# Performance work log

Hardware: AMD Instinct MI355X
Metric: run time of the kernel (lower is better)

## Reference

```python
import jax, jax.numpy as jnp
import numpy as np

HEADS = 8


def setup_inputs() -> dict:
    key = jax.random.key(0)
    ks = jax.random.split(key, 12)
    B, H, W, C = 2, 128, 256, 256
    inner = C  # num_heads * dim_head = 8 * 32

    def p(k, shape):
        return jax.random.normal(k, shape, dtype=jnp.float32) * 0.02

    return {
        "x": jax.random.normal(ks[0], (B, H * W, C), dtype=jnp.float32),
        "Wq_h": p(ks[1], (C, inner)),
        "Wk_h": p(ks[2], (C, inner)),
        "Wv_h": p(ks[3], (C, inner)),
        "Wo_h": p(ks[4], (inner, C)),
        "bo_h": p(ks[5], (C,)),
        "Wq_w": p(ks[6], (C, inner)),
        "Wk_w": p(ks[7], (C, inner)),
        "Wv_w": p(ks[8], (C, inner)),
        "Wo_w": p(ks[9], (inner, C)),
        "bo_w": p(ks[10], (C,)),
        "h": H,
        "w": W,
    }


def reference(x, Wq_h, Wk_h, Wv_h, Wo_h, bo_h, Wq_w, Wk_w, Wv_w, Wo_w, bo_w, h, w):
    b, n, c = x.shape
    heads = HEADS
    d = Wq_h.shape[1] // heads  # dim_head
    scale = d ** -0.5
    xs = x.reshape(b, h, w, c)  # [B,H,W,C]

    def proj(Wm):
        # [B,H,W,heads,d]
        return (xs @ Wm).reshape(b, h, w, heads, d)

    # --- height-axis attention: each column attends across all rows ---
    q, k, v = proj(Wq_h), proj(Wk_h), proj(Wv_h)
    s = jnp.einsum('bxwnd,bywnd->bwnxy', q, k) * scale  # [B,W,heads,H,H]
    a = jax.nn.softmax(s, axis=-1)
    oh = jnp.einsum('bwnxy,bywnd->bxwnd', a, v).reshape(b, h, w, heads * d)
    oh = oh @ Wo_h + bo_h

    # --- width-axis attention: each row attends across all columns ---
    q, k, v = proj(Wq_w), proj(Wk_w), proj(Wv_w)
    s = jnp.einsum('bhxnd,bhynd->bhnxy', q, k) * scale  # [B,H,heads,W,W]
    a = jax.nn.softmax(s, axis=-1)
    ow = jnp.einsum('bhnxy,bhynd->bhxnd', a, v).reshape(b, h, w, heads * d)
    ow = ow @ Wo_w + bo_w

    return (oh + ow).reshape(b, n, c)
```

## Files before the change

### kernel.cpp

```cpp
#include <hip/hip_runtime.h>
#include <hip/hip_bf16.h>
#include <stdint.h>

typedef unsigned short u16;
typedef short bf16x8 __attribute__((ext_vector_type(8)));
typedef float f32x4  __attribute__((ext_vector_type(4)));
typedef float f32x16 __attribute__((ext_vector_type(16)));
typedef unsigned int u32x4 __attribute__((ext_vector_type(4)));

__device__ __forceinline__ u16 f2bf(float f) {
    uint32_t u = __builtin_bit_cast(uint32_t, f);
    u += 0x7fffu + ((u >> 16) & 1u);
    return (u16)(u >> 16);
}

#if __has_builtin(__builtin_amdgcn_exp2f)
#define EXP2(x) __builtin_amdgcn_exp2f(x)
#else
extern "C" __device__ float __ocml_native_exp2_f32(float);
#define EXP2(x) __ocml_native_exp2_f32(x)
#endif

__device__ __forceinline__ void gl_lds16(const u16* g, u16* l) {
    __builtin_amdgcn_global_load_lds(
        (__attribute__((address_space(1))) void*)(g),
        (__attribute__((address_space(3))) void*)(l),
        16, 0, 0);
}

#define MM 65536
#define CC 256

#define QSCALE (1.4426950408889634f * 0.17677669529663687f)

__device__ __forceinline__ int perm_h(int t) {
    return ((t >> 15) << 15) | ((t & 127) << 8) | ((t >> 7) & 255);
}


__global__ void prep_kernel(
    const float* __restrict__ Wq_h, const float* __restrict__ Wk_h, const float* __restrict__ Wv_h,
    const float* __restrict__ Wo_h, const float* __restrict__ bo_h,
    const float* __restrict__ Wq_w, const float* __restrict__ Wk_w, const float* __restrict__ Wv_w,
    const float* __restrict__ Wo_w, const float* __restrict__ bo_w,
    u16* __restrict__ Wh_t, u16* __restrict__ Ww_t,
    u16* __restrict__ Woh_t, u16* __restrict__ Wow_t,
    u16* __restrict__ Wocat, float* __restrict__ bias)
{
    const int tid = blockIdx.x * 256 + threadIdx.x;
    const int nth = gridDim.x * 256;

    for (int i = tid; i < 768 * 256; i += nth) {
        int n = i >> 8, kk = i & 255;
        int which = n >> 8, nn = n & 255;
        const float* Wsh = (which == 0) ? Wq_h : (which == 1) ? Wk_h : Wv_h;
        const float* Wsw = (which == 0) ? Wq_w : (which == 1) ? Wk_w : Wv_w;
        Wh_t[i] = f2bf(Wsh[kk * 256 + nn]);
        Ww_t[i] = f2bf(Wsw[kk * 256 + nn]);
    }
    for (int i = tid; i < 256 * 256; i += nth) {
        int n = i >> 8, k = i & 255;
        Woh_t[i] = f2bf(Wo_h[k * 256 + n]);
        Wow_t[i] = f2bf(Wo_w[k * 256 + n]);
    }
    for (int i = tid; i < 256 * 512; i += nth) {
        int n = i >> 9, k = i & 511;
        float v = (k < 256) ? Wo_h[k * 256 + n] : Wo_w[(k - 256) * 256 + n];
        Wocat[i] = f2bf(v);
    }
    for (int i = tid; i < 256; i += nth) bias[i] = bo_h[i] + bo_w[i];
}

__global__ __launch_bounds__(256) void xcvt_kernel(const float* __restrict__ x, u16* __restrict__ xb)
{
    int i = blockIdx.x * 256 + threadIdx.x;
    const int nth = gridDim.x * 256;
    const int total = MM * 256 / 8;
    for (; i < total; i += nth) {
        const float* ap = x + (size_t)i * 8;
        float4 f0 = *(const float4*)ap;
        float4 f1 = *(const float4*)(ap + 4);
        u16 o[8] = { f2bf(f0.x), f2bf(f0.y), f2bf(f0.z), f2bf(f0.w),
                     f2bf(f1.x), f2bf(f1.y), f2bf(f1.z), f2bf(f1.w) };
        *(int4*)(xb + (size_t)i * 8) = *(const int4*)o;
    }
}

template<int PH, int XB>
__global__ __launch_bounds__(256) void gemm_qk_kernel(
    const float* __restrict__ x, const u16* __restrict__ xb, const u16* __restrict__ Bt,
    u16* __restrict__ Qb, u16* __restrict__ Kb)
{
    constexpr int S = PH ? 128 : 256;
    constexpr int L = PH ? 7 : 8;
    const int K = 256;
    __shared__ u16 sh[XB ? 32768 : 16384];
    const int tid = threadIdx.x;
    const int lane = tid & 63, wave = tid >> 6;
    const int wm = wave & 1, wn = wave >> 1;
    const int l15 = lane & 15, lq = lane >> 4;

    const int id = blockIdx.x;
    const int xcd = id & 7, wq = id >> 3;
    const int mt = xcd * 64 + (wq >> 2), nt = wq & 3;
    const int m0 = mt * 128, n0 = nt * 128;

    f32x4 acc[4][4];
#pragma unroll
    for (int i = 0; i < 4; i++)
#pragma unroll
        for (int j = 0; j < 4; j++)
#pragma unroll
            for (int t = 0; t < 4; t++) acc[i][j][t] = 0.0f;

    auto mma_tile = [&](const u16* As, const u16* Bs) {
#pragma unroll
        for (int ks = 0; ks < 2; ks++) {
            bf16x8 af[4], bfr[4];
#pragma unroll
            for (int i = 0; i < 4; i++) {
                int row = wm * 64 + i * 16 + l15;
                int ca  = ks * 4 + lq;
                af[i]  = *(const bf16x8*)(As + row * 64 + ((ca ^ (row & 7)) << 3));
                int nn  = wn * 64 + i * 16 + l15;
                bfr[i] = *(const bf16x8*)(Bs + nn * 64 + ((ca ^ (nn & 7)) << 3));
            }
#pragma unroll
            for (int i = 0; i < 4; i++)
#pragma unroll
                for (int j = 0; j < 4; j++)
                    acc[i][j] = __builtin_amdgcn_mfma_f32_16x16x32_bf16(af[i], bfr[j], acc[i][j], 0, 0, 0);
        }
    };

    if constexpr (XB) {
        u16* As_[2] = { sh,        sh + 16384 };
        u16* Bs_[2] = { sh + 8192, sh + 24576 };
        auto stage = [&](int kt, int buf) {
#pragma unroll
            for (int i = 0; i < 4; i++) {
                int cid = i * 256 + tid;
                int r = cid >> 3, sc = cid & 7;
                int gk = kt + ((sc ^ (r & 7)) << 3);
                int rm = PH ? perm_h(m0 + r) : (m0 + r);
                gl_lds16(xb + (size_t)rm * 256 + gk, As_[buf] + cid * 8);
                gl_lds16(Bt + (size_t)(n0 + r) * K + gk, Bs_[buf] + cid * 8);
            }
        };
        stage(0, 0);
        __syncthreads();
#pragma unroll
        for (int t = 0; t < 4; t++) {
            if (t + 1 < 4) stage((t + 1) * 64, (t + 1) & 1);
            mma_tile(As_[t & 1], Bs_[t & 1]);
            __syncthreads();
        }
    } else {
        u16* As = sh;
        u16* Bs = sh + 8192;
        for (int kt = 0; kt < K; kt += 64) {
            __syncthreads();
#pragma unroll
            for (int i = 0; i < 4; i++) {
                int cid = i * 256 + tid;
                int r = cid >> 3, sc = cid & 7;
                int gk = kt + ((sc ^ (r & 7)) << 3);
                int rm = PH ? perm_h(m0 + r) : (m0 + r);
                const float* ap = x + (size_t)rm * 256 + gk;
                float4 f0 = *(const float4*)ap;
                float4 f1 = *(const float4*)(ap + 4);
                u16 o[8] = { f2bf(f0.x), f2bf(f0.y), f2bf(f0.z), f2bf(f0.w),
                             f2bf(f1.x), f2bf(f1.y), f2bf(f1.z), f2bf(f1.w) };
                *(int4*)(As + (size_t)cid * 8) = *(const int4*)o;
                *(int4*)(Bs + (size_t)cid * 8) = *(const int4*)(Bt + (size_t)(n0 + r) * K + gk);
            }
            __syncthreads();
            mma_tile(As, Bs);
        }
        __syncthreads();
    }

    const float scale = (nt < 2) ? (float)QSCALE : 1.0f;
#pragma unroll
    for (int i = 0; i < 4; i++)
#pragma unroll
        for (int j = 0; j < 4; j++)
#pragma unroll
            for (int r = 0; r < 4; r++) {
                int row = wm * 64 + i * 16 + lq * 4 + r;
                int col = wn * 64 + j * 16 + l15;
                sh[row * 128 + (col ^ ((row & 7) << 3))] = f2bf(acc[i][j][r] * scale);
            }
    __syncthreads();

    u16* dstb = (nt < 2) ? Qb : Kb;
    const int head = (nt * 4 + wave) & 7;
    const int gi = m0 >> L;
    const int seqbase = m0 & (S - 1);
    u16* dst = dstb + ((size_t)(gi * 8 + head) * S + seqbase) * 32;
    const int ln_ = lane & 31, lh_ = lane >> 5;
#pragma unroll
    for (int qt = 0; qt < 4; qt++)
#pragma unroll
        for (int half = 0; half < 2; half++) {
            int row  = qt * 32 + ln_;
            int colb = wave * 32 + half * 16 + lh_ * 8;
            int4 v = *(const int4*)(sh + row * 128 + (colb ^ ((row & 7) << 3)));
            *(int4*)(dst + qt * 1024 + half * 512 + lane * 8) = v;
        }
}

template<int PH, int XB>
__global__ __launch_bounds__(256) void gemm_vt_kernel(
    const u16* __restrict__ Wt, const float* __restrict__ x, const u16* __restrict__ xb,
    u16* __restrict__ Vb)
{
    constexpr int S = PH ? 128 : 256;
    const int K = 256;
    __shared__ u16 sh[XB ? 32768 : 16384];
    const int tid = threadIdx.x;
    const int lane = tid & 63, wave = tid >> 6;
    const int wm = wave & 1, wn = wave >> 1;
    const int l15 = lane & 15, lq = lane >> 4;
    const int m0 = blockIdx.y * 128, n0 = blockIdx.x * 128;

    f32x4 acc[4][4];
#pragma unroll
    for (int i = 0; i < 4; i++)
#pragma unroll
        for (int j = 0; j < 4; j++)
#pragma unroll
            for (int t = 0; t < 4; t++) acc[i][j][t] = 0.0f;

    auto mma_tile = [&](const u16* As, const u16* Bs) {
#pragma unroll
        for (int ks = 0; ks < 2; ks++) {
            bf16x8 af[4], bfr[4];
#pragma unroll
            for (int i = 0; i < 4; i++) {
                int row = wm * 64 + i * 16 + l15;
                int ca  = ks * 4 + lq;
                af[i]  = *(const bf16x8*)(As + row * 64 + ((ca ^ (row & 7)) << 3));
                int nn  = wn * 64 + i * 16 + l15;
                bfr[i] = *(const bf16x8*)(Bs + nn * 64 + ((ca ^ (nn & 7)) << 3));
            }
#pragma unroll
            for (int i = 0; i < 4; i++)
#pragma unroll
                for (int j = 0; j < 4; j++)
                    acc[i][j] = __builtin_amdgcn_mfma_f32_16x16x32_bf16(af[i], bfr[j], acc[i][j], 0, 0, 0);
        }
    };

    if constexpr (XB) {
        u16* As_[2] = { sh,        sh + 16384 };
        u16* Bs_[2] = { sh + 8192, sh + 24576 };
        auto stage = [&](int kt, int buf) {
#pragma unroll
            for (int i = 0; i < 4; i++) {
                int cid = i * 256 + tid;
                int r = cid >> 3, sc = cid & 7;
                int gk = kt + ((sc ^ (r & 7)) << 3);
                gl_lds16(Wt + (size_t)(m0 + r) * K + gk, As_[buf] + cid * 8);
                int cm = PH ? perm_h(n0 + r) : (n0 + r);
                gl_lds16(xb + (size_t)cm * 256 + gk, Bs_[buf] + cid * 8);
            }
        };
        stage(0, 0);
        __syncthreads();
#pragma unroll
        for (int t = 0; t < 4; t++) {
            if (t + 1 < 4) stage((t + 1) * 64, (t + 1) & 1);
            mma_tile(As_[t & 1], Bs_[t & 1]);
            __syncthreads();
        }
    } else {
        u16* As = sh;
        u16* Bs = sh + 8192;
        for (int kt = 0; kt < K; kt += 64) {
            __syncthreads();
#pragma unroll
            for (int i = 0; i < 4; i++) {
                int cid = i * 256 + tid;
                int r = cid >> 3, sc = cid & 7;
                int gk = kt + ((sc ^ (r & 7)) << 3);
                *(int4*)(As + (size_t)cid * 8) = *(const int4*)(Wt + (size_t)(m0 + r) * K + gk);
                int cm = PH ? perm_h(n0 + r) : (n0 + r);
                const float* bp = x + (size_t)cm * 256 + gk;
                float4 f0 = *(const float4*)bp;
                float4 f1 = *(const float4*)(bp + 4);
                u16 o[8] = { f2bf(f0.x), f2bf(f0.y), f2bf(f0.z), f2bf(f0.w),
                             f2bf(f1.x), f2bf(f1.y), f2bf(f1.z), f2bf(f1.w) };
                *(int4*)(Bs + (size_t)cid * 8) = *(const int4*)o;
            }
            __syncthreads();
            mma_tile(As, Bs);
        }
        __syncthreads();
    }

#pragma unroll
    for (int i = 0; i < 4; i++)
#pragma unroll
        for (int j = 0; j < 4; j++)
#pragma unroll
            for (int r = 0; r < 4; r++) {
                int row = wm * 64 + i * 16 + lq * 4 + r;
                int col = wn * 64 + j * 16 + l15;
                sh[row * 128 + (col ^ ((row & 7) << 3))] = f2bf(acc[i][j][r]);
            }
    __syncthreads();

    const int gi = n0 >> (PH ? 7 : 8);
    const int seqbase = n0 & (S - 1);
    const int head = (m0 >> 5) + wave;
    u16* dst = Vb + ((size_t)(gi * 8 + head) * S + seqbase) * 32;
    const int ln_ = lane & 31, lh_ = lane >> 5;
#pragma unroll
    for (int cl = 0; cl < 4; cl++)
#pragma unroll
        for (int half = 0; half < 2; half++) {
            int row  = wave * 32 + ln_;
            int colb = cl * 32 + half * 16 + lh_ * 8;
            int4 v = *(const int4*)(sh + row * 128 + (colb ^ ((row & 7) << 3)));
            *(int4*)(dst + cl * 1024 + half * 512 + lane * 8) = v;
        }
}

__global__ __launch_bounds__(256) void gemm_out_fused_kernel(
    const u16* __restrict__ Ah, const u16* __restrict__ Aw,
    const u16* __restrict__ Bcat, float* __restrict__ Cout, const float* __restrict__ bias)
{
    const int K = 512, N = 256;
    __shared__ u16 sh[32768];
    const int tid = threadIdx.x;
    const int lane = tid & 63, wave = tid >> 6;
    const int wm = wave & 1, wn = wave >> 1;
    const int l15 = lane & 15, lq = lane >> 4;

    const int id = blockIdx.x;
    const int xcd = id & 7, wq = id >> 3;
    const int mt = xcd * 64 + (wq >> 1), nt = wq & 1;
    const int m0 = mt * 128, n0 = nt * 128;

    f32x4 acc[4][4];
#pragma unroll
    for (int i = 0; i < 4; i++)
#pragma unroll
        for (int j = 0; j < 4; j++)
#pragma unroll
            for (int t = 0; t < 4; t++) acc[i][j][t] = 0.0f;

    u16* As_[2] = { sh,        sh + 16384 };
    u16* Bs_[2] = { sh + 8192, sh + 24576 };
    auto stage = [&](int kt, int buf) {
        const u16* Abase = (kt < 256) ? Ah : Aw;
        int koff = kt & 255;
#pragma unroll
        for (int i = 0; i < 4; i++) {
            int cid = i * 256 + tid;
            int r = cid >> 3, sc = cid & 7;
            int gs = (sc ^ (r & 7)) << 3;
            gl_lds16(Abase + (size_t)(m0 + r) * 256 + koff + gs, As_[buf] + cid * 8);
            gl_lds16(Bcat + (size_t)(n0 + r) * K + kt + gs, Bs_[buf] + cid * 8);
        }
    };

    stage(0, 0);
    __syncthreads();
#pragma unroll
    for (int t = 0; t < 8; t++) {
        if (t + 1 < 8) stage((t + 1) * 64, (t + 1) & 1);
        const u16* As = As_[t & 1];
        const u16* Bs = Bs_[t & 1];
#pragma unroll
        for (int ks = 0; ks < 2; ks++) {
            bf16x8 af[4], bfr[4];
#pragma unroll
            for (int i = 0; i < 4; i++) {
                int row = wm * 64 + i * 16 + l15;
                int ca  = ks * 4 + lq;
                af[i]  = *(const bf16x8*)(As + row * 64 + ((ca ^ (row & 7)) << 3));
                int nn  = wn * 64 + i * 16 + l15;
                bfr[i] = *(const bf16x8*)(Bs + nn * 64 + ((ca ^ (nn & 7)) << 3));
            }
#pragma unroll
            for (int i = 0; i < 4; i++)
#pragma unroll
                for (int j = 0; j < 4; j++)
                    acc[i][j] = __builtin_amdgcn_mfma_f32_16x16x32_bf16(af[i], bfr[j], acc[i][j], 0, 0, 0);
        }
        __syncthreads();
    }
#pragma unroll
    for (int i = 0; i < 4; i++)
#pragma unroll
        for (int j = 0; j < 4; j++)
#pragma unroll
            for (int r = 0; r < 4; r++) {
                int row = m0 + wm * 64 + i * 16 + lq * 4 + r;
                int col = n0 + wn * 64 + j * 16 + l15;
                Cout[(size_t)row * N + col] = acc[i][j][r] + bias[col];
            }
}

template<int MODE>
__global__ __launch_bounds__(256) void gemm_out_kernel(
    const u16* __restrict__ A16, const u16* __restrict__ Bt,
    float* __restrict__ Cout, const float* __restrict__ bias)
{
    const int K = 256, N = 256;
    __shared__ u16 As[128 * 64];
    __shared__ u16 Bs[128 * 64];
    const int tid = threadIdx.x;
    const int lane = tid & 63, wave = tid >> 6;
    const int wm = wave & 1, wn = wave >> 1;
    const int l15 = lane & 15, lq = lane >> 4;
    const int m0 = blockIdx.y * 128, n0 = blockIdx.x * 128;

    f32x4 acc[4][4];
#pragma unroll
    for (int i = 0; i < 4; i++)
#pragma unroll
        for (int j = 0; j < 4; j++)
#pragma unroll
            for (int t = 0; t < 4; t++) acc[i][j][t] = 0.0f;

    for (int kt = 0; kt < K; kt += 64) {
        __syncthreads();
#pragma unroll
        for (int i = 0; i < 4; i++) {
            int cid = i * 256 + tid;
            int r = cid >> 3, sc = cid & 7;
            int gk = kt + ((sc ^ (r & 7)) << 3);
            *(int4*)(As + (size_t)cid * 8) = *(const int4*)(A16 + (size_t)(m0 + r) * K + gk);
            *(int4*)(Bs + (size_t)cid * 8) = *(const int4*)(Bt + (size_t)(n0 + r) * K + gk);
        }
        __syncthreads();
#pragma unroll
        for (int ks = 0; ks < 2; ks++) {
            bf16x8 af[4], bfr[4];
#pragma unroll
            for (int i = 0; i < 4; i++) {
                int row = wm * 64 + i * 16 + l15;
                int ca  = ks * 4 + lq;
                af[i]  = *(const bf16x8*)(As + row * 64 + ((ca ^ (row & 7)) << 3));
                int nn  = wn * 64 + i * 16 + l15;
                bfr[i] = *(const bf16x8*)(Bs + nn * 64 + ((ca ^ (nn & 7)) << 3));
            }
#pragma unroll
            for (int i = 0; i < 4; i++)
#pragma unroll
                for (int j = 0; j < 4; j++)
                    acc[i][j] = __builtin_amdgcn_mfma_f32_16x16x32_bf16(af[i], bfr[j], acc[i][j], 0, 0, 0);
        }
    }
#pragma unroll
    for (int i = 0; i < 4; i++)
#pragma unroll
        for (int j = 0; j < 4; j++)
#pragma unroll
            for (int r = 0; r < 4; r++) {
                int row = m0 + wm * 64 + i * 16 + lq * 4 + r;
                int col = n0 + wn * 64 + j * 16 + l15;
                size_t idx = (size_t)row * N + col;
                if (MODE == 1) Cout[idx] = acc[i][j][r] + bias[col];
                else           Cout[idx] += acc[i][j][r];
            }
}

template<int S, int PH, int NT>
__global__ __launch_bounds__(NT) void attn_kernel(
    const u16* __restrict__ Qb, const u16* __restrict__ Kb,
    const u16* __restrict__ Vb, u16* __restrict__ att)
{
    constexpr int NC = S / 32;
    const int tid = threadIdx.x;
    const int lane = tid & 63;
    const int wave = tid >> 6;
    const int ln = lane & 31;
    const int lh = lane >> 5;

    const int bid = blockIdx.x;
    const int head = bid & 7;
    const int gi = bid >> 3;
    const int qs = wave * 32;
    const int g = gi * 8 + head;

    const u16* Qg = Qb + (size_t)g * S * 32;
    const u16* Kg = Kb + (size_t)g * S * 32;
    const u16* Vg = Vb + (size_t)g * S * 32;

    const u16* qp = Qg + (qs >> 5) * 1024 + lane * 8;
    bf16x8 bq0 = *(const bf16x8*)qp;
    bf16x8 bq1 = *(const bf16x8*)(qp + 512);

    f32x16 kz;
#pragma unroll
    for (int t = 0; t < 16; t++) kz[t] = 0.0f;
    asm("" : "+v"(kz));

    float rs[4] = {0.0f, 0.0f, 0.0f, 0.0f};
    f32x16 oacc;
#pragma unroll
    for (int t = 0; t < 16; t++) oacc[t] = 0.0f;

    const u16* kp0 = Kg + lane * 8;
    const u16* vp0 = Vg + lane * 8;
    bf16x8 ak0 = *(const bf16x8*)kp0;
    bf16x8 ak1 = *(const bf16x8*)(kp0 + 512);
    bf16x8 bv0 = *(const bf16x8*)vp0;
    bf16x8 bv1 = *(const bf16x8*)(vp0 + 512);

    for (int c = 0; c < NC; c++) {
        f32x16 z = __builtin_amdgcn_mfma_f32_32x32x16_bf16(ak0, bq0, kz, 0, 0, 0);
        z = __builtin_amdgcn_mfma_f32_32x32x16_bf16(ak1, bq1, z, 0, 0, 0);

        int cn = (c + 1 < NC) ? c + 1 : c;
        const u16* kp = kp0 + cn * 1024;
        const u16* vp = vp0 + cn * 1024;
        bf16x8 nk0 = *(const bf16x8*)kp;
        bf16x8 nk1 = *(const bf16x8*)(kp + 512);
        bf16x8 nv0 = *(const bf16x8*)vp;
        bf16x8 nv1 = *(const bf16x8*)(vp + 512);

        asm("" : "+v"(z));
        float p[16];
#pragma unroll
        for (int r = 0; r < 16; r++) { p[r] = EXP2(z[r]); rs[r & 3] += p[r]; }

        unsigned w[8];
#pragma unroll
        for (int t = 0; t < 8; t++) {
            unsigned d;
            asm("v_cvt_pk_bf16_f32 %0, %1, %2" : "=v"(d) : "v"(p[2 * t]), "v"(p[2 * t + 1]));
            w[t] = d;
        }
        auto s0 = __builtin_amdgcn_permlane32_swap(w[0], w[2], false, false);
        auto s1 = __builtin_amdgcn_permlane32_swap(w[1], w[3], false, false);
        auto s2 = __builtin_amdgcn_permlane32_swap(w[4], w[6], false, false);
        auto s3 = __builtin_amdgcn_permlane32_swap(w[5], w[7], false, false);
        u32x4 a0 = { (unsigned)s0[0], (unsigned)s1[0], (unsigned)s0[1], (unsigned)s1[1] };
        u32x4 a1 = { (unsigned)s2[0], (unsigned)s3[0], (unsigned)s2[1], (unsigned)s3[1] };
        bf16x8 pa0 = __builtin_bit_cast(bf16x8, a0);
        bf16x8 pa1 = __builtin_bit_cast(bf16x8, a1);

        oacc = __builtin_amdgcn_mfma_f32_32x32x16_bf16(pa0, bv0, oacc, 0, 0, 0);
        oacc = __builtin_amdgcn_mfma_f32_32x32x16_bf16(pa1, bv1, oacc, 0, 0, 0);

        ak0 = nk0; ak1 = nk1; bv0 = nv0; bv1 = nv1;
    }

    float rsum = (rs[0] + rs[1]) + (rs[2] + rs[3]);
    rsum += __shfl_xor(rsum, 32);
    float inv = 1.0f / rsum;
#pragma unroll
    for (int r = 0; r < 16; r++) {
        int row = (r & 3) + ((r >> 2) << 3) + (lh << 2);
        float is = __shfl(inv, row);
        int seq = qs + row;
        int m = PH ? ((gi >> 8) * 32768 + seq * 256 + (gi & 255))
                   : (gi * 256 + seq);
        att[(size_t)m * 256 + head * 32 + ln] = f2bf(oacc[r] * is);
    }
}

extern "C" void kernel_launch(void* const* d_in, const int* in_sizes, int n_in,
                              void* d_out, int out_size, void* d_ws, size_t ws_size,
                              hipStream_t stream)
{
    (void)in_sizes; (void)n_in; (void)out_size;
    const float* x    = (const float*)d_in[0];
    const float* Wq_h = (const float*)d_in[1];
    const float* Wk_h = (const float*)d_in[2];
    const float* Wv_h = (const float*)d_in[3];
    const float* Wo_h = (const float*)d_in[4];
    const float* bo_h = (const float*)d_in[5];
    const float* Wq_w = (const float*)d_in[6];
    const float* Wk_w = (const float*)d_in[7];
    const float* Wv_w = (const float*)d_in[8];
    const float* Wo_w = (const float*)d_in[9];
    const float* bo_w = (const float*)d_in[10];

    const size_t NB = (size_t)MM * 256;
    u16* Qb   = (u16*)d_ws;
    u16* Kb   = Qb + NB;
    u16* Vb   = Kb + NB;
    u16* attb = Vb + NB;
    u16* xb   = attb + NB;
    const size_t WT = (size_t)2 * 768 * 256 + (size_t)2 * 256 * 256 + (size_t)256 * 512 + 512;
    const bool use_xb = ws_size >= (5 * NB + WT) * sizeof(u16);
    u16* wp = use_xb ? (xb + NB) : xb;
    u16* Wh_t  = wp;
    u16* Ww_t  = Wh_t + 768 * 256;
    u16* Woh_t = Ww_t + 768 * 256;
    u16* Wow_t = Woh_t + 256 * 256;
    u16* Wocat = Wow_t + 256 * 256;
    float* bias = (float*)(Wocat + 256 * 512);

    prep_kernel<<<512, 256, 0, stream>>>(Wq_h, Wk_h, Wv_h, Wo_h, bo_h,
                                         Wq_w, Wk_w, Wv_w, Wo_w, bo_w,
                                         Wh_t, Ww_t, Woh_t, Wow_t, Wocat, bias);
    if (use_xb)
        xcvt_kernel<<<8192, 256, 0, stream>>>(x, xb);

    if (use_xb) {
        gemm_qk_kernel<1, 1><<<2048, 256, 0, stream>>>(x, xb, Wh_t, Qb, Kb);
        gemm_vt_kernel<1, 1><<<dim3(512, 2), 256, 0, stream>>>(Wh_t + 512 * 256, x, xb, Vb);
        attn_kernel<128, 1, 256><<<4096, 256, 0, stream>>>(Qb, Kb, Vb, attb);

        gemm_qk_kernel<0, 1><<<2048, 256, 0, stream>>>(x, xb, Ww_t, Qb, Kb);
        gemm_vt_kernel<0, 1><<<dim3(512, 2), 256, 0, stream>>>(Ww_t + 512 * 256, x, xb, Vb);
        attn_kernel<256, 0, 512><<<2048, 512, 0, stream>>>(Qb, Kb, Vb, xb);

        gemm_out_fused_kernel<<<1024, 256, 0, stream>>>(attb, xb, Wocat,
                                                        (float*)d_out, bias);
    } else {
        gemm_qk_kernel<1, 0><<<2048, 256, 0, stream>>>(x, xb, Wh_t, Qb, Kb);
        gemm_vt_kernel<1, 0><<<dim3(512, 2), 256, 0, stream>>>(Wh_t + 512 * 256, x, xb, Vb);
        attn_kernel<128, 1, 256><<<4096, 256, 0, stream>>>(Qb, Kb, Vb, attb);
        gemm_out_kernel<1><<<dim3(2, 512), 256, 0, stream>>>(attb, Woh_t, (float*)d_out, bias);

        gemm_qk_kernel<0, 0><<<2048, 256, 0, stream>>>(x, xb, Ww_t, Qb, Kb);
        gemm_vt_kernel<0, 0><<<dim3(512, 2), 256, 0, stream>>>(Ww_t + 512 * 256, x, xb, Vb);
        attn_kernel<256, 0, 512><<<2048, 512, 0, stream>>>(Qb, Kb, Vb, attb);
        gemm_out_kernel<2><<<dim3(2, 512), 256, 0, stream>>>(attb, Wow_t, (float*)d_out, nullptr);
    }
}
```

Measured before the change: 318.6 us.

## Use 256x128 tiles with 512-thread blocks in QK and output GEMMs

The QK projection GEMM and the fused output GEMM now use 512-thread blocks (8 waves) that compute 256x128 output tiles, so each B tile staged in LDS serves twice as many rows and the grid is halved. The double-buffered LDS pipeline is replaced by a single buffer with a sync before and after each stage. The QK epilogue now writes back in two passes through LDS because of the larger tile. Loss of load/compute overlap and larger blocks may reduce latency hiding.

Measured after the change: 334.8 us. 1.05x slower.

```diff
diff --git a/kernel.cpp b/kernel.cpp
--- a/kernel.cpp
+++ b/kernel.cpp
@@ -87,23 +87,25 @@
 }
 
 template<int PH, int XB>
-__global__ __launch_bounds__(256) void gemm_qk_kernel(
+__global__ __launch_bounds__(512) void gemm_qk_kernel(
     const float* __restrict__ x, const u16* __restrict__ xb, const u16* __restrict__ Bt,
     u16* __restrict__ Qb, u16* __restrict__ Kb)
 {
     constexpr int S = PH ? 128 : 256;
     constexpr int L = PH ? 7 : 8;
     const int K = 256;
-    __shared__ u16 sh[XB ? 32768 : 16384];
+    __shared__ u16 sh[24576];
+    u16* As = sh;
+    u16* Bs = sh + 16384;
     const int tid = threadIdx.x;
     const int lane = tid & 63, wave = tid >> 6;
-    const int wm = wave & 1, wn = wave >> 1;
+    const int wm = wave >> 1, wn = wave & 1;
     const int l15 = lane & 15, lq = lane >> 4;
 
     const int id = blockIdx.x;
     const int xcd = id & 7, wq = id >> 3;
-    const int mt = xcd * 64 + (wq >> 2), nt = wq & 3;
-    const int m0 = mt * 128, n0 = nt * 128;
+    const int mt = xcd * 32 + (wq >> 2), nt = wq & 3;
+    const int m0 = mt * 256, n0 = nt * 128;
 
     f32x4 acc[4][4];
 #pragma unroll
@@ -113,56 +115,28 @@
 #pragma unroll
             for (int t = 0; t < 4; t++) acc[i][j][t] = 0.0f;
 
-    auto mma_tile = [&](const u16* As, const u16* Bs) {
-#pragma unroll
-        for (int ks = 0; ks < 2; ks++) {
-            bf16x8 af[4], bfr[4];
-#pragma unroll
-            for (int i = 0; i < 4; i++) {
-                int row = wm * 64 + i * 16 + l15;
-                int ca  = ks * 4 + lq;
-                af[i]  = *(const bf16x8*)(As + row * 64 + ((ca ^ (row & 7)) << 3));
-                int nn  = wn * 64 + i * 16 + l15;
-                bfr[i] = *(const bf16x8*)(Bs + nn * 64 + ((ca ^ (nn & 7)) << 3));
-            }
-#pragma unroll
-            for (int i = 0; i < 4; i++)
-#pragma unroll
-                for (int j = 0; j < 4; j++)
-                    acc[i][j] = __builtin_amdgcn_mfma_f32_16x16x32_bf16(af[i], bfr[j], acc[i][j], 0, 0, 0);
-        }
-    };
-
-    if constexpr (XB) {
-        u16* As_[2] = { sh,        sh + 16384 };
-        u16* Bs_[2] = { sh + 8192, sh + 24576 };
-        auto stage = [&](int kt, int buf) {
-#pragma unroll
-            for (int i = 0; i < 4; i++) {
-                int cid = i * 256 + tid;
+    for (int kt = 0; kt < K; kt += 64) {
+        __syncthreads();
+        if constexpr (XB) {
+#pragma unroll
+            for (int i = 0; i < 4; i++) {
+                int cid = i * 512 + tid;
                 int r = cid >> 3, sc = cid & 7;
                 int gk = kt + ((sc ^ (r & 7)) << 3);
                 int rm = PH ? perm_h(m0 + r) : (m0 + r);
-                gl_lds16(xb + (size_t)rm * 256 + gk, As_[buf] + cid * 8);
-                gl_lds16(Bt + (size_t)(n0 + r) * K + gk, Bs_[buf] + cid * 8);
-            }
-        };
-        stage(0, 0);
-        __syncthreads();
-#pragma unroll
-        for (int t = 0; t < 4; t++) {
-            if (t + 1 < 4) stage((t + 1) * 64, (t + 1) & 1);
-            mma_tile(As_[t & 1], Bs_[t & 1]);
-            __syncthreads();
-        }
-    } else {
-        u16* As = sh;
-        u16* Bs = sh + 8192;
-        for (int kt = 0; kt < K; kt += 64) {
-            __syncthreads();
-#pragma unroll
-            for (int i = 0; i < 4; i++) {
-                int cid = i * 256 + tid;
+                gl_lds16(xb + (size_t)rm * 256 + gk, As + cid * 8);
+            }
+#pragma unroll
+            for (int i = 0; i < 2; i++) {
+                int cid = i * 512 + tid;
+                int r = cid >> 3, sc = cid & 7;
+                int gk = kt + ((sc ^ (r & 7)) << 3);
+                gl_lds16(Bt + (size_t)(n0 + r) * K + gk, Bs + cid * 8);
+            }
+        } else {
+#pragma unroll
+            for (int i = 0; i < 4; i++) {
+                int cid = i * 512 + tid;
                 int r = cid >> 3, sc = cid & 7;
                 int gk = kt + ((sc ^ (r & 7)) << 3);
                 int rm = PH ? perm_h(m0 + r) : (m0 + r);
@@ -172,42 +146,70 @@
                 u16 o[8] = { f2bf(f0.x), f2bf(f0.y), f2bf(f0.z), f2bf(f0.w),
                              f2bf(f1.x), f2bf(f1.y), f2bf(f1.z), f2bf(f1.w) };
                 *(int4*)(As + (size_t)cid * 8) = *(const int4*)o;
+            }
+#pragma unroll
+            for (int i = 0; i < 2; i++) {
+                int cid = i * 512 + tid;
+                int r = cid >> 3, sc = cid & 7;
+                int gk = kt + ((sc ^ (r & 7)) << 3);
                 *(int4*)(Bs + (size_t)cid * 8) = *(const int4*)(Bt + (size_t)(n0 + r) * K + gk);
             }
-            __syncthreads();
-            mma_tile(As, Bs);
-        }
-        __syncthreads();
+        }
+        __syncthreads();
+#pragma unroll
+        for (int ks = 0; ks < 2; ks++) {
+            bf16x8 af[4], bfr[4];
+#pragma unroll
+            for (int i = 0; i < 4; i++) {
+                int row = wm * 64 + i * 16 + l15;
+                int ca  = ks * 4 + lq;
+                af[i]  = *(const bf16x8*)(As + row * 64 + ((ca ^ (row & 7)) << 3));
+                int nn  = wn * 64 + i * 16 + l15;
+                bfr[i] = *(const bf16x8*)(Bs + nn * 64 + ((ca ^ (nn & 7)) << 3));
+            }
+#pragma unroll
+            for (int i = 0; i < 4; i++)
+#pragma unroll
+                for (int j = 0; j < 4; j++)
+                    acc[i][j] = __builtin_amdgcn_mfma_f32_16x16x32_bf16(af[i], bfr[j], acc[i][j], 0, 0, 0);
+        }
     }
 
     const float scale = (nt < 2) ? (float)QSCALE : 1.0f;
-#pragma unroll
-    for (int i = 0; i < 4; i++)
-#pragma unroll
-        for (int j = 0; j < 4; j++)
-#pragma unroll
-            for (int r = 0; r < 4; r++) {
-                int row = wm * 64 + i * 16 + lq * 4 + r;
-                int col = wn * 64 + j * 16 + l15;
-                sh[row * 128 + (col ^ ((row & 7) << 3))] = f2bf(acc[i][j][r] * scale);
-            }
-    __syncthreads();
-
     u16* dstb = (nt < 2) ? Qb : Kb;
-    const int head = (nt * 4 + wave) & 7;
-    const int gi = m0 >> L;
-    const int seqbase = m0 & (S - 1);
-    u16* dst = dstb + ((size_t)(gi * 8 + head) * S + seqbase) * 32;
     const int ln_ = lane & 31, lh_ = lane >> 5;
-#pragma unroll
-    for (int qt = 0; qt < 4; qt++)
-#pragma unroll
-        for (int half = 0; half < 2; half++) {
+    const int hg = wave & 3;
+    const int half = wave >> 2;
+    const int head = (nt & 1) * 4 + hg;
+
+#pragma unroll
+    for (int p = 0; p < 2; p++) {
+        __syncthreads();
+        if ((wm >> 1) == p) {
+#pragma unroll
+            for (int i = 0; i < 4; i++)
+#pragma unroll
+                for (int j = 0; j < 4; j++)
+#pragma unroll
+                    for (int r = 0; r < 4; r++) {
+                        int row = (wm & 1) * 64 + i * 16 + lq * 4 + r;
+                        int col = wn * 64 + j * 16 + l15;
+                        sh[row * 128 + (col ^ ((row & 7) << 3))] = f2bf(acc[i][j][r] * scale);
+                    }
+        }
+        __syncthreads();
+        int base = m0 + p * 128;
+        int gi = base >> L;
+        int seqbase = base & (S - 1);
+        u16* dst = dstb + ((size_t)(gi * 8 + head) * S + seqbase) * 32;
+#pragma unroll
+        for (int qt = 0; qt < 4; qt++) {
             int row  = qt * 32 + ln_;
-            int colb = wave * 32 + half * 16 + lh_ * 8;
+            int colb = hg * 32 + half * 16 + lh_ * 8;
             int4 v = *(const int4*)(sh + row * 128 + (colb ^ ((row & 7) << 3)));
             *(int4*)(dst + qt * 1024 + half * 512 + lane * 8) = v;
         }
+    }
 }
 
 template<int PH, int XB>
@@ -327,21 +329,23 @@
         }
 }
 
-__global__ __launch_bounds__(256) void gemm_out_fused_kernel(
+__global__ __launch_bounds__(512) void gemm_out_fused_kernel(
     const u16* __restrict__ Ah, const u16* __restrict__ Aw,
     const u16* __restrict__ Bcat, float* __restrict__ Cout, const float* __restrict__ bias)
 {
     const int K = 512, N = 256;
-    __shared__ u16 sh[32768];
+    __shared__ u16 sh[24576];
+    u16* As = sh;
+    u16* Bs = sh + 16384;
     const int tid = threadIdx.x;
     const int lane = tid & 63, wave = tid >> 6;
-    const int wm = wave & 1, wn = wave >> 1;
+    const int wm = wave >> 1, wn = wave & 1;
     const int l15 = lane & 15, lq = lane >> 4;
 
     const int id = blockIdx.x;
     const int xcd = id & 7, wq = id >> 3;
-    const int mt = xcd * 64 + (wq >> 1), nt = wq & 1;
-    const int m0 = mt * 128, n0 = nt * 128;
+    const int mt = xcd * 32 + (wq >> 1), nt = wq & 1;
+    const int m0 = mt * 256, n0 = nt * 128;
 
     f32x4 acc[4][4];
 #pragma unroll
@@ -351,28 +355,25 @@
 #pragma unroll
             for (int t = 0; t < 4; t++) acc[i][j][t] = 0.0f;
 
-    u16* As_[2] = { sh,        sh + 16384 };
-    u16* Bs_[2] = { sh + 8192, sh + 24576 };
-    auto stage = [&](int kt, int buf) {
+    for (int kt = 0; kt < K; kt += 64) {
+        __syncthreads();
         const u16* Abase = (kt < 256) ? Ah : Aw;
         int koff = kt & 255;
 #pragma unroll
         for (int i = 0; i < 4; i++) {
-            int cid = i * 256 + tid;
+            int cid = i * 512 + tid;
             int r = cid >> 3, sc = cid & 7;
             int gs = (sc ^ (r & 7)) << 3;
-            gl_lds16(Abase + (size_t)(m0 + r) * 256 + koff + gs, As_[buf] + cid * 8);
-            gl_lds16(Bcat + (size_t)(n0 + r) * K + kt + gs, Bs_[buf] + cid * 8);
-        }
-    };
-
-    stage(0, 0);
-    __syncthreads();
-#pragma unroll
-    for (int t = 0; t < 8; t++) {
-        if (t + 1 < 8) stage((t + 1) * 64, (t + 1) & 1);
-        const u16* As = As_[t & 1];
-        const u16* Bs = Bs_[t & 1];
+            gl_lds16(Abase + (size_t)(m0 + r) * 256 + koff + gs, As + cid * 8);
+        }
+#pragma unroll
+        for (int i = 0; i < 2; i++) {
+            int cid = i * 512 + tid;
+            int r = cid >> 3, sc = cid & 7;
+            int gs = (sc ^ (r & 7)) << 3;
+            gl_lds16(Bcat + (size_t)(n0 + r) * K + kt + gs, Bs + cid * 8);
+        }
+        __syncthreads();
 #pragma unroll
         for (int ks = 0; ks < 2; ks++) {
             bf16x8 af[4], bfr[4];
@@ -390,7 +391,6 @@
                 for (int j = 0; j < 4; j++)
                     acc[i][j] = __builtin_amdgcn_mfma_f32_16x16x32_bf16(af[i], bfr[j], acc[i][j], 0, 0, 0);
         }
-        __syncthreads();
     }
 #pragma unroll
     for (int i = 0; i < 4; i++)
@@ -605,23 +605,23 @@
         xcvt_kernel<<<8192, 256, 0, stream>>>(x, xb);
 
     if (use_xb) {
-        gemm_qk_kernel<1, 1><<<2048, 256, 0, stream>>>(x, xb, Wh_t, Qb, Kb);
+        gemm_qk_kernel<1, 1><<<1024, 512, 0, stream>>>(x, xb, Wh_t, Qb, Kb);
         gemm_vt_kernel<1, 1><<<dim3(512, 2), 256, 0, stream>>>(Wh_t + 512 * 256, x, xb, Vb);
         attn_kernel<128, 1, 256><<<4096, 256, 0, stream>>>(Qb, Kb, Vb, attb);
 
-        gemm_qk_kernel<0, 1><<<2048, 256, 0, stream>>>(x, xb, Ww_t, Qb, Kb);
+        gemm_qk_kernel<0, 1><<<1024, 512, 0, stream>>>(x, xb, Ww_t, Qb, Kb);
         gemm_vt_kernel<0, 1><<<dim3(512, 2), 256, 0, stream>>>(Ww_t + 512 * 256, x, xb, Vb);
         attn_kernel<256, 0, 512><<<2048, 512, 0, stream>>>(Qb, Kb, Vb, xb);
 
-        gemm_out_fused_kernel<<<1024, 256, 0, stream>>>(attb, xb, Wocat,
-                                                        (float*)d_out, bias);
+        gemm_out_fused_kernel<<<512, 512, 0, stream>>>(attb, xb, Wocat,
+                                                       (float*)d_out, bias);
     } else {
-        gemm_qk_kernel<1, 0><<<2048, 256, 0, stream>>>(x, xb, Wh_t, Qb, Kb);
+        gemm_qk_kernel<1, 0><<<1024, 512, 0, stream>>>(x, xb, Wh_t, Qb, Kb);
         gemm_vt_kernel<1, 0><<<dim3(512, 2), 256, 0, stream>>>(Wh_t + 512 * 256, x, xb, Vb);
         attn_kernel<128, 1, 256><<<4096, 256, 0, stream>>>(Qb, Kb, Vb, attb);
         gemm_out_kernel<1><<<dim3(2, 512), 256, 0, stream>>>(attb, Woh_t, (float*)d_out, bias);
 
-        gemm_qk_kernel<0, 0><<<2048, 256, 0, stream>>>(x, xb, Ww_t, Qb, Kb);
+        gemm_qk_kernel<0, 0><<<1024, 512, 0, stream>>>(x, xb, Ww_t, Qb, Kb);
         gemm_vt_kernel<0, 0><<<dim3(512, 2), 256, 0, stream>>>(Ww_t + 512 * 256, x, xb, Vb);
         attn_kernel<256, 0, 512><<<2048, 512, 0, stream>>>(Qb, Kb, Vb, attb);
         gemm_out_kernel<2><<<dim3(2, 512), 256, 0, stream>>>(attb, Wow_t, (float*)d_out, nullptr);
```
